# Optimization experiments

Measured on AMD Instinct MI355X. Metric: run time of the kernel, lower is better.

## Reference

```python
import jax, jax.numpy as jnp
import numpy as np
from jax import lax

NUM_CNNS = 300
INPUT_LEN = 608
NUM_CLASSES = 50
FILTER = 19
POOL = 7
HIDDEN = 100
BATCH = 256
L_CONV = INPUT_LEN - FILTER + 1          # 590
L_POOL = (L_CONV - POOL) // POOL + 1     # 84
EPS = 1e-5


def setup_inputs() -> dict:
    key = jax.random.key(0)
    ks = jax.random.split(key, 24)
    U, H = NUM_CNNS, HIDDEN
    d = {}
    d["x"] = jax.random.normal(ks[0], (BATCH, 4, INPUT_LEN), dtype=jnp.float32)
    # conv1: grouped Conv1d(4*U -> U, k=19, groups=U) on replicated input == dense Conv1d(4 -> U)
    d["w1"] = jax.random.normal(ks[1], (U, 4, FILTER), dtype=jnp.float32) * 0.1
    d["b1"] = jax.random.normal(ks[2], (U,), dtype=jnp.float32) * 0.05
    d["g1"] = jax.random.uniform(ks[3], (U,), dtype=jnp.float32, minval=0.5, maxval=1.5)
    d["be1"] = jax.random.normal(ks[4], (U,), dtype=jnp.float32) * 0.05
    d["m1"] = jax.random.normal(ks[5], (U,), dtype=jnp.float32) * 0.05
    d["v1"] = jax.random.uniform(ks[6], (U,), dtype=jnp.float32, minval=0.5, maxval=1.5)
    # grouped 1x1 conv: per-unit Linear 84 -> 100
    d["w2"] = jax.random.normal(ks[7], (U, H, L_POOL), dtype=jnp.float32) * (1.0 / np.sqrt(L_POOL))
    d["b2"] = jax.random.normal(ks[8], (U, H), dtype=jnp.float32) * 0.05
    d["g2"] = jax.random.uniform(ks[9], (U, H), dtype=jnp.float32, minval=0.5, maxval=1.5)
    d["be2"] = jax.random.normal(ks[10], (U, H), dtype=jnp.float32) * 0.05
    d["m2"] = jax.random.normal(ks[11], (U, H), dtype=jnp.float32) * 0.05
    d["v2"] = jax.random.uniform(ks[12], (U, H), dtype=jnp.float32, minval=0.5, maxval=1.5)
    # grouped 1x1 conv: per-unit Linear 100 -> 1
    d["w3"] = jax.random.normal(ks[13], (U, H), dtype=jnp.float32) * (1.0 / np.sqrt(H))
    d["b3"] = jax.random.normal(ks[14], (U,), dtype=jnp.float32) * 0.05
    d["g3"] = jax.random.uniform(ks[15], (U,), dtype=jnp.float32, minval=0.5, maxval=1.5)
    d["be3"] = jax.random.normal(ks[16], (U,), dtype=jnp.float32) * 0.05
    d["m3"] = jax.random.normal(ks[17], (U,), dtype=jnp.float32) * 0.05
    d["v3"] = jax.random.uniform(ks[18], (U,), dtype=jnp.float32, minval=0.5, maxval=1.5)
    # final Linear(U -> num_classes)
    d["wf"] = jax.random.normal(ks[19], (NUM_CLASSES, U), dtype=jnp.float32) * (1.0 / np.sqrt(U))
    d["bf"] = jax.random.normal(ks[20], (NUM_CLASSES,), dtype=jnp.float32) * 0.05
    return d


def _bn(y, g, be, m, v):
    return (y - m) * (g * lax.rsqrt(v + EPS)) + be


def reference(x, w1, b1, g1, be1, m1, v1, w2, b2, g2, be2, m2, v2,
              w3, b3, g3, be3, m3, v3, wf, bf):
    # conv1 (replicate + grouped conv == dense conv over 4 channels)
    y = lax.conv_general_dilated(x, w1, window_strides=(1,), padding='VALID',
                                 dimension_numbers=('NCH', 'OIH', 'NCH'))  # [B,U,590]
    y = y + b1[None, :, None]
    y = _bn(y, g1[None, :, None], be1[None, :, None], m1[None, :, None], v1[None, :, None])
    y = jnp.exp(y)  # ExpActivation
    # MaxPool1d(7,7): 590 -> 84 (uses first 588 positions)
    B = y.shape[0]
    y = y[:, :, :L_POOL * POOL].reshape(B, NUM_CNNS, L_POOL, POOL).max(axis=-1)  # [B,U,84]
    # per-unit MLP 84 -> 100 (grouped 1x1 conv) + BN + ReLU (dropout is eval-mode identity)
    h = jnp.einsum('buf,uof->buo', y, w2) + b2[None]  # [B,U,100]
    h = _bn(h, g2[None], be2[None], m2[None], v2[None])
    h = jax.nn.relu(h)
    # per-unit 100 -> 1 + BN + ReLU
    z = jnp.einsum('buo,uo->bu', h, w3) + b3[None]  # [B,U]
    z = _bn(z, g3[None], be3[None], m3[None], v3[None])
    z = jax.nn.relu(z)
    # final Linear
    return z @ wf.T + bf
```

## Files before the change

kernel.cpp:

```cpp
#include <hip/hip_runtime.h>
#include <hip/hip_bf16.h>

#define BATCH    256
#define NU       300
#define LIN      608
#define FILT     19
#define LPOOL    84
#define POOL     7
#define HID      100
#define NCLS     50
#define EPS      1e-5f
#define KP       96
#define NP       112
#define LDK      104
#define WROW     104
#define WBROWS   320
#define TCHUNK   112
#define MTN      19
#define CSTR     116

typedef __attribute__((ext_vector_type(8))) short short8;
typedef __attribute__((ext_vector_type(4))) float float4v;
typedef __attribute__((ext_vector_type(4))) unsigned short us4;

#define LDS_WAIT() __asm__ __volatile__("s_waitcnt lgkmcnt(0)" ::: "memory")

__device__ __forceinline__ unsigned short f2bf(float f) {
    unsigned u = __float_as_uint(f);
    u += 0x7fffu + ((u >> 16) & 1u);
    return (unsigned short)(u >> 16);
}
__device__ __forceinline__ float bf2f(unsigned short h) {
    return __uint_as_float(((unsigned)h) << 16);
}

__global__ void k_prep(const float* __restrict__ w1, const float* __restrict__ x,
                       const float* __restrict__ b1, const float* __restrict__ g1,
                       const float* __restrict__ be1, const float* __restrict__ m1,
                       const float* __restrict__ v1, const float* __restrict__ w2,
                       unsigned short* __restrict__ Wbh,
                       unsigned short* __restrict__ Wbl,
                       unsigned int* __restrict__ xc,
                       float2* __restrict__ s1c1,
                       unsigned short* __restrict__ w2c)
{
    const int idx = blockIdx.x * 256 + threadIdx.x;
    const int NW = WBROWS * WROW;
    if (idx < NW) {
        const int u = idx / WROW, kk = idx - u * WROW;
        float wv = 0.f;
        if (u < NU && kk < 96) {
            const int c = kk / 24, tap = kk - 24 * c;
            if (tap < FILT) wv = w1[(u * 4 + c) * FILT + tap];
        }
        const unsigned short hi = f2bf(wv);
        Wbh[idx] = hi;
        Wbl[idx] = f2bf(wv - bf2f(hi));
    }
    const int j = idx - NW;
    if (j >= 0 && j < BATCH * 4 * LIN) {
        const float xv = x[j];
        const unsigned short hi = f2bf(xv);
        const unsigned short lo = f2bf(xv - bf2f(hi));
        xc[j] = (unsigned)hi | ((unsigned)lo << 16);
    }
    const int j2 = j - BATCH * 4 * LIN;
    if (j2 >= 0 && j2 < MTN * 16) {
        float2 v = {0.f, 0.f};
        if (j2 < NU) {
            const float s = g1[j2] * rsqrtf(v1[j2] + EPS);
            v.x = s;
            v.y = (b1[j2] - m1[j2]) * s + be1[j2];
        }
        s1c1[j2] = v;
    }
    const int j3 = j2 - MTN * 16;
    if (j3 >= 0 && j3 < NU * NP * LDK) {
        const int u  = j3 / (NP * LDK);
        const int r  = j3 - u * (NP * LDK);
        const int o  = r / LDK;
        const int kc = r - o * LDK;
        float wv = 0.f;
        if (o < HID && kc < LPOOL) wv = w2[((size_t)u * HID + o) * LPOOL + kc];
        w2c[j3] = f2bf(wv);
    }
}

__global__ __launch_bounds__(256, 3)
void k_conv7d(const unsigned short* __restrict__ Wbh,
              const unsigned short* __restrict__ Wbl,
              const unsigned int* __restrict__ xc,
              const float2* __restrict__ s1c1,
              unsigned short* __restrict__ ypool)
{
    __shared__ __align__(16) unsigned short Bh[TCHUNK * LDK];
    __shared__ __align__(16) float Cs[4][16 * CSTR];

    const int tid = threadIdx.x;
    const int b   = blockIdx.x;
    const int tc  = blockIdx.y;
    const int t0  = TCHUNK * tc;
    const int NT  = (tc == 5) ? 2 : 7;

    for (int i = tid; i < TCHUNK * 12; i += 256) {
        const int trow = i / 12;
        if (trow >= 16 * NT) continue;
        const int rem   = i - 12 * trow;
        const int c     = rem / 3;
        const int third = rem - 3 * c;
        const int kkb   = 24 * c + 8 * third;
        const int tt0   = t0 + trow + 8 * third;
        const unsigned int* src = xc + ((b * 4 + c) * LIN + tt0);

        unsigned int w[8];
        if (third < 2 && tt0 + 8 <= LIN) {
            const uint4 v0 = *(const uint4*)(src);
            const uint4 v1 = *(const uint4*)(src + 4);
            w[0] = v0.x; w[1] = v0.y; w[2] = v0.z; w[3] = v0.w;
            w[4] = v1.x; w[5] = v1.y; w[6] = v1.z; w[7] = v1.w;
        } else {
#pragma unroll
            for (int j = 0; j < 8; ++j) {
                const int tap = 8 * third + j;
                const int tt  = tt0 + j;
                unsigned int v = 0;
                if (tap < FILT && tt < LIN) v = src[j];
                w[j] = v;
            }
        }
        short8 hv;
#pragma unroll
        for (int j = 0; j < 8; ++j) hv[j] = (short)(w[j] & 0xffffu);
        *(short8*)(&Bh[trow * LDK + kkb]) = hv;
    }
    __syncthreads();

    const int lane = tid & 63;
    const int n    = lane & 15;
    const int quad = lane >> 4;
    const int wave = tid >> 6;
    float* Csw = Cs[wave];

    const int u_l = lane & 15;
    const int wq  = lane >> 4;
    const int pg0 = 16 * tc + 4 * wq;

    const int jend = 5 * wave + ((wave == 3) ? 4 : 5);
    for (int mt0 = 5 * wave; mt0 < jend; mt0 += 2) {
        const bool two = (mt0 + 1 < jend);

        short8 a0h[3], a0l[3], a1h[3], a1l[3];
        {
            const unsigned short* wrh = Wbh + (size_t)(mt0 * 16 + n) * WROW;
            const unsigned short* wrl = Wbl + (size_t)(mt0 * 16 + n) * WROW;
#pragma unroll
            for (int s = 0; s < 3; ++s) {
                a0h[s] = *(const short8*)(wrh + 32 * s + 8 * quad);
                a0l[s] = *(const short8*)(wrl + 32 * s + 8 * quad);
            }
            const int m1r = two ? (mt0 + 1) : mt0;
            const unsigned short* wrh1 = Wbh + (size_t)(m1r * 16 + n) * WROW;
            const unsigned short* wrl1 = Wbl + (size_t)(m1r * 16 + n) * WROW;
#pragma unroll
            for (int s = 0; s < 3; ++s) {
                a1h[s] = *(const short8*)(wrh1 + 32 * s + 8 * quad);
                a1l[s] = *(const short8*)(wrl1 + 32 * s + 8 * quad);
            }
        }

        float4v acc[2][7];
#pragma unroll
        for (int t2 = 0; t2 < 2; ++t2)
#pragma unroll
            for (int nt = 0; nt < 7; ++nt)
                acc[t2][nt] = (float4v){0.f, 0.f, 0.f, 0.f};

#pragma unroll
        for (int nt = 0; nt < 7; ++nt) {
            if (nt < NT) {
                short8 bhf[3];
#pragma unroll
                for (int s = 0; s < 3; ++s)
                    bhf[s] = *(const short8*)(&Bh[(16 * nt + n) * LDK + 32 * s + 8 * quad]);
#pragma unroll
                for (int s = 0; s < 3; ++s)
                    acc[0][nt] = __builtin_amdgcn_mfma_f32_16x16x32_bf16(
                        bhf[s], a0h[s], acc[0][nt], 0, 0, 0);
#pragma unroll
                for (int s = 0; s < 3; ++s)
                    acc[0][nt] = __builtin_amdgcn_mfma_f32_16x16x32_bf16(
                        bhf[s], a0l[s], acc[0][nt], 0, 0, 0);
                if (two) {
#pragma unroll
                    for (int s = 0; s < 3; ++s)
                        acc[1][nt] = __builtin_amdgcn_mfma_f32_16x16x32_bf16(
                            bhf[s], a1h[s], acc[1][nt], 0, 0, 0);
#pragma unroll
                    for (int s = 0; s < 3; ++s)
                        acc[1][nt] = __builtin_amdgcn_mfma_f32_16x16x32_bf16(
                            bhf[s], a1l[s], acc[1][nt], 0, 0, 0);
                }
            }
        }

#pragma unroll
        for (int t2 = 0; t2 < 2; ++t2) {
            if (t2 == 1 && !two) break;
            const int mt = mt0 + t2;

            LDS_WAIT();
#pragma unroll
            for (int nt = 0; nt < 7; ++nt) {
                if (nt < NT)
                    *(float4v*)(&Csw[n * CSTR + 16 * nt + 4 * quad]) = acc[t2][nt];
            }
            LDS_WAIT();

            float rv[28];
#pragma unroll
            for (int r7 = 0; r7 < 7; ++r7)
                *(float4v*)(&rv[4 * r7]) =
                    *(const float4v*)(&Csw[u_l * CSTR + 28 * wq + 4 * r7]);

            const int uglob = mt * 16 + u_l;
            const float2 sc = s1c1[uglob];
            us4 pk;
#pragma unroll
            for (int w4 = 0; w4 < 4; ++w4) {
                const int pg = pg0 + w4;
                unsigned short ov = 0;
                if (pg < LPOOL) {
                    float m0 = fmaxf(rv[7 * w4 + 0], rv[7 * w4 + 1]);
                    float m1 = fmaxf(rv[7 * w4 + 2], rv[7 * w4 + 3]);
                    float m2 = fmaxf(rv[7 * w4 + 4], rv[7 * w4 + 5]);
                    m0 = fmaxf(m0, rv[7 * w4 + 6]);
                    ov = f2bf(__expf(fmaf(fmaxf(fmaxf(m0, m1), m2), sc.x, sc.y)));
                }
                pk[w4] = ov;
            }
            if (uglob < NU)
                *(us4*)(&ypool[((size_t)b * NU + uglob) * KP + pg0]) = pk;
        }
    }
}

__global__ __launch_bounds__(256, 4)
void k_mlp(const unsigned short* __restrict__ ypool,
           const unsigned short* __restrict__ w2c,
           const float* __restrict__ g2, const float* __restrict__ b2,
           const float* __restrict__ be2, const float* __restrict__ m2,
           const float* __restrict__ v2,
           const float* __restrict__ w3, const float* __restrict__ b3,
           const float* __restrict__ g3, const float* __restrict__ be3,
           const float* __restrict__ m3, const float* __restrict__ v3,
           float* __restrict__ zbuf)
{
    __shared__ __align__(16) float4 cs4[NP];

    const int tid = threadIdx.x;
    const int u   = blockIdx.x;
    const int b0  = blockIdx.y * 64;

    if (tid < NP) {
        float4 cv = {0.f, 0.f, 0.f, 0.f};
        if (tid < HID) {
            const int uo = u * HID + tid;
            const float s = g2[uo] * rsqrtf(v2[uo] + EPS);
            cv.x = s;
            cv.y = (b2[uo] - m2[uo]) * s + be2[uo];
            cv.z = w3[uo];
        }
        cs4[tid] = cv;
    }
    __syncthreads();

    const int lane = tid & 63;
    const int wave = tid >> 6;
    const int col  = lane & 15;
    const int quad = lane >> 4;
    const int bb   = b0 + 16 * wave + col;

    short8 bf_[3];
    {
        const unsigned short* yrow = ypool + ((size_t)bb * NU + u) * KP;
#pragma unroll
        for (int s = 0; s < 3; ++s)
            bf_[s] = *(const short8*)(yrow + 32 * s + 8 * quad);
    }

    const unsigned short* wbase = w2c + (size_t)u * (NP * LDK);
    float zp = 0.f;
#pragma unroll
    for (int mt = 0; mt < 7; ++mt) {
        short8 af[3];
#pragma unroll
        for (int s = 0; s < 3; ++s)
            af[s] = *(const short8*)(wbase + (16 * mt + col) * LDK + 32 * s + 8 * quad);

        float4v a0 = {0.f, 0.f, 0.f, 0.f};
#pragma unroll
        for (int s = 0; s < 3; ++s)
            a0 = __builtin_amdgcn_mfma_f32_16x16x32_bf16(af[s], bf_[s], a0, 0, 0, 0);
#pragma unroll
        for (int r = 0; r < 4; ++r) {
            const float4 cv = cs4[16 * mt + 4 * quad + r];
            zp = fmaf(fmaxf(fmaf(a0[r], cv.x, cv.y), 0.f), cv.z, zp);
        }
    }

    zp += __shfl_xor(zp, 16);
    zp += __shfl_xor(zp, 32);

    if (quad == 0) {
        const float s3 = g3[u] * rsqrtf(v3[u] + EPS);
        const float c3 = (b3[u] - m3[u]) * s3 + be3[u];
        zbuf[(size_t)u * BATCH + bb] = fmaxf(fmaf(zp, s3, c3), 0.f);
    }
}

__global__ __launch_bounds__(256, 4)
void k_final(const float* __restrict__ zbuf, const float* __restrict__ wf,
             const float* __restrict__ bf, float* __restrict__ out)
{
    __shared__ float red[4][64];
    const int nc   = blockIdx.x;
    const int bq   = blockIdx.y;
    const int lane = threadIdx.x & 63;
    const int wave = threadIdx.x >> 6;
    const int b    = bq * 64 + lane;

    float a0 = 0.f, a1 = 0.f, a2 = 0.f;
    const int u0 = wave * 75;
#pragma unroll 5
    for (int i = 0; i < 75; i += 3) {
        a0 = fmaf(zbuf[(size_t)(u0 + i + 0) * BATCH + b], wf[nc * NU + u0 + i + 0], a0);
        a1 = fmaf(zbuf[(size_t)(u0 + i + 1) * BATCH + b], wf[nc * NU + u0 + i + 1], a1);
        a2 = fmaf(zbuf[(size_t)(u0 + i + 2) * BATCH + b], wf[nc * NU + u0 + i + 2], a2);
    }
    red[wave][lane] = (a0 + a1) + a2;
    __syncthreads();
    if (threadIdx.x < 64) {
        const float s = (red[0][lane] + red[1][lane]) + (red[2][lane] + red[3][lane]);
        out[(size_t)b * NCLS + nc] = s + bf[nc];
    }
}

extern "C" void kernel_launch(void* const* d_in, const int* in_sizes, int n_in,
                              void* d_out, int out_size, void* d_ws, size_t ws_size,
                              hipStream_t stream)
{
    const float* x   = (const float*)d_in[0];
    const float* w1  = (const float*)d_in[1];
    const float* b1  = (const float*)d_in[2];
    const float* g1  = (const float*)d_in[3];
    const float* be1 = (const float*)d_in[4];
    const float* m1  = (const float*)d_in[5];
    const float* v1  = (const float*)d_in[6];
    const float* w2  = (const float*)d_in[7];
    const float* b2  = (const float*)d_in[8];
    const float* g2  = (const float*)d_in[9];
    const float* be2 = (const float*)d_in[10];
    const float* m2  = (const float*)d_in[11];
    const float* v2  = (const float*)d_in[12];
    const float* w3  = (const float*)d_in[13];
    const float* b3  = (const float*)d_in[14];
    const float* g3  = (const float*)d_in[15];
    const float* be3 = (const float*)d_in[16];
    const float* m3  = (const float*)d_in[17];
    const float* v3  = (const float*)d_in[18];
    const float* wf  = (const float*)d_in[19];
    const float* bf  = (const float*)d_in[20];

    unsigned short* ypool = (unsigned short*)d_ws;
    float* zbuf = (float*)((char*)d_ws + 14745600);
    unsigned short* Wbh = (unsigned short*)((char*)d_ws + 15052800);
    unsigned short* Wbl = (unsigned short*)((char*)d_ws + 15119360);
    unsigned int*   xc  = (unsigned int*)((char*)d_ws + 15185920);
    float2*         sc1 = (float2*)((char*)d_ws + 17676288);
    unsigned short* w2c = (unsigned short*)((char*)d_ws + 17678720);

    const int prep_elems = WBROWS * WROW + BATCH * 4 * LIN + MTN * 16 + NU * NP * LDK;
    k_prep<<<(prep_elems + 255) / 256, 256, 0, stream>>>(
        w1, x, b1, g1, be1, m1, v1, w2, Wbh, Wbl, xc, sc1, w2c);

    dim3 gc(BATCH, 6);
    k_conv7d<<<gc, 256, 0, stream>>>(Wbh, Wbl, xc, sc1, ypool);

    dim3 gm(NU, BATCH / 64);
    k_mlp<<<gm, 256, 0, stream>>>(ypool, w2c, g2, b2, be2, m2, v2,
                                  w3, b3, g3, be3, m3, v3, zbuf);

    dim3 gf(NCLS, 4);
    k_final<<<gf, 256, 0, stream>>>(zbuf, wf, bf, (float*)d_out);
}
```

Measured before the change: 150.7 us.

## Reuse w2 fragments across two batch tiles in MLP kernel, tighten w2 layout

The MLP kernel now processes 128 batch rows per block instead of 64. Each loaded weight fragment feeds two MFMA chains, which halves the global reads of the per-unit w2 tile, and the grid shrinks to 600 blocks. The packed w2 row stride is reduced from 104 to 96 to cut prep writes and the memory footprint. The conv kernel's staging loop is reindexed plane-major so consecutive threads read consecutive time rows, which should coalesce better. In exchange the MLP kernel uses more registers per thread and runs fewer blocks.

```diff
diff --git a/kernel.cpp b/kernel.cpp
--- a/kernel.cpp
+++ b/kernel.cpp
@@ -13,6 +13,7 @@
 #define KP       96
 #define NP       112
 #define LDK      104
+#define LDKW     96
 #define WROW     104
 #define WBROWS   320
 #define TCHUNK   112
@@ -75,11 +76,11 @@
         s1c1[j2] = v;
     }
     const int j3 = j2 - MTN * 16;
-    if (j3 >= 0 && j3 < NU * NP * LDK) {
-        const int u  = j3 / (NP * LDK);
-        const int r  = j3 - u * (NP * LDK);
-        const int o  = r / LDK;
-        const int kc = r - o * LDK;
+    if (j3 >= 0 && j3 < NU * NP * LDKW) {
+        const int u  = j3 / (NP * LDKW);
+        const int r  = j3 - u * (NP * LDKW);
+        const int o  = r / LDKW;
+        const int kc = r - o * LDKW;
         float wv = 0.f;
         if (o < HID && kc < LPOOL) wv = w2[((size_t)u * HID + o) * LPOOL + kc];
         w2c[j3] = f2bf(wv);
@@ -102,12 +103,12 @@
     const int t0  = TCHUNK * tc;
     const int NT  = (tc == 5) ? 2 : 7;
 
-    for (int i = tid; i < TCHUNK * 12; i += 256) {
-        const int trow = i / 12;
+    for (int i = tid; i < 12 * TCHUNK; i += 256) {
+        const int plane = i / TCHUNK;
+        const int trow  = i - plane * TCHUNK;
         if (trow >= 16 * NT) continue;
-        const int rem   = i - 12 * trow;
-        const int c     = rem / 3;
-        const int third = rem - 3 * c;
+        const int third = plane >> 2;
+        const int c     = plane & 3;
         const int kkb   = 24 * c + 8 * third;
         const int tt0   = t0 + trow + 8 * third;
         const unsigned int* src = xc + ((b * 4 + c) * LIN + tt0);
@@ -259,7 +260,7 @@
 
     const int tid = threadIdx.x;
     const int u   = blockIdx.x;
-    const int b0  = blockIdx.y * 64;
+    const int b0  = blockIdx.y * 128;
 
     if (tid < NP) {
         float4 cv = {0.f, 0.f, 0.f, 0.f};
@@ -278,43 +279,51 @@
     const int wave = tid >> 6;
     const int col  = lane & 15;
     const int quad = lane >> 4;
-    const int bb   = b0 + 16 * wave + col;
-
-    short8 bf_[3];
+    const int bbA  = b0 + 16 * wave + col;
+    const int bbB  = bbA + 64;
+
+    short8 bfA[3], bfB[3];
     {
-        const unsigned short* yrow = ypool + ((size_t)bb * NU + u) * KP;
-#pragma unroll
-        for (int s = 0; s < 3; ++s)
-            bf_[s] = *(const short8*)(yrow + 32 * s + 8 * quad);
-    }
-
-    const unsigned short* wbase = w2c + (size_t)u * (NP * LDK);
-    float zp = 0.f;
+        const unsigned short* yrA = ypool + ((size_t)bbA * NU + u) * KP;
+        const unsigned short* yrB = ypool + ((size_t)bbB * NU + u) * KP;
+#pragma unroll
+        for (int s = 0; s < 3; ++s) {
+            bfA[s] = *(const short8*)(yrA + 32 * s + 8 * quad);
+            bfB[s] = *(const short8*)(yrB + 32 * s + 8 * quad);
+        }
+    }
+
+    const unsigned short* wbase = w2c + (size_t)u * (NP * LDKW);
+    float zpA = 0.f, zpB = 0.f;
 #pragma unroll
     for (int mt = 0; mt < 7; ++mt) {
         short8 af[3];
 #pragma unroll
         for (int s = 0; s < 3; ++s)
-            af[s] = *(const short8*)(wbase + (16 * mt + col) * LDK + 32 * s + 8 * quad);
-
-        float4v a0 = {0.f, 0.f, 0.f, 0.f};
-#pragma unroll
-        for (int s = 0; s < 3; ++s)
-            a0 = __builtin_amdgcn_mfma_f32_16x16x32_bf16(af[s], bf_[s], a0, 0, 0, 0);
+            af[s] = *(const short8*)(wbase + (16 * mt + col) * LDKW + 32 * s + 8 * quad);
+
+        float4v a0 = {0.f, 0.f, 0.f, 0.f}, a1 = {0.f, 0.f, 0.f, 0.f};
+#pragma unroll
+        for (int s = 0; s < 3; ++s) {
+            a0 = __builtin_amdgcn_mfma_f32_16x16x32_bf16(af[s], bfA[s], a0, 0, 0, 0);
+            a1 = __builtin_amdgcn_mfma_f32_16x16x32_bf16(af[s], bfB[s], a1, 0, 0, 0);
+        }
 #pragma unroll
         for (int r = 0; r < 4; ++r) {
             const float4 cv = cs4[16 * mt + 4 * quad + r];
-            zp = fmaf(fmaxf(fmaf(a0[r], cv.x, cv.y), 0.f), cv.z, zp);
-        }
-    }
-
-    zp += __shfl_xor(zp, 16);
-    zp += __shfl_xor(zp, 32);
+            zpA = fmaf(fmaxf(fmaf(a0[r], cv.x, cv.y), 0.f), cv.z, zpA);
+            zpB = fmaf(fmaxf(fmaf(a1[r], cv.x, cv.y), 0.f), cv.z, zpB);
+        }
+    }
+
+    zpA += __shfl_xor(zpA, 16); zpA += __shfl_xor(zpA, 32);
+    zpB += __shfl_xor(zpB, 16); zpB += __shfl_xor(zpB, 32);
 
     if (quad == 0) {
         const float s3 = g3[u] * rsqrtf(v3[u] + EPS);
         const float c3 = (b3[u] - m3[u]) * s3 + be3[u];
-        zbuf[(size_t)u * BATCH + bb] = fmaxf(fmaf(zp, s3, c3), 0.f);
+        zbuf[(size_t)u * BATCH + bbA] = fmaxf(fmaf(zpA, s3, c3), 0.f);
+        zbuf[(size_t)u * BATCH + bbB] = fmaxf(fmaf(zpB, s3, c3), 0.f);
     }
 }
 
@@ -379,14 +388,14 @@
     float2*         sc1 = (float2*)((char*)d_ws + 17676288);
     unsigned short* w2c = (unsigned short*)((char*)d_ws + 17678720);
 
-    const int prep_elems = WBROWS * WROW + BATCH * 4 * LIN + MTN * 16 + NU * NP * LDK;
+    const int prep_elems = WBROWS * WROW + BATCH * 4 * LIN + MTN * 16 + NU * NP * LDKW;
     k_prep<<<(prep_elems + 255) / 256, 256, 0, stream>>>(
         w1, x, b1, g1, be1, m1, v1, w2, Wbh, Wbl, xc, sc1, w2c);
 
     dim3 gc(BATCH, 6);
     k_conv7d<<<gc, 256, 0, stream>>>(Wbh, Wbl, xc, sc1, ypool);
 
-    dim3 gm(NU, BATCH / 64);
+    dim3 gm(NU, 2);
     k_mlp<<<gm, 256, 0, stream>>>(ypool, w2c, g2, b2, be2, m2, v2,
                                   w3, b3, g3, be3, m3, v3, zbuf);
 
```

Measured after the change: 148.8 us (median of 2 runs). About the same (-1.3%).

## Fuse prep conversions into conv and MLP kernels, batch all rows per MLP block

Applied to the files above, without the earlier changes.

Removes the separate prep kernel that converted x, w1, w2 and the BN1 constants into bf16 workspace buffers. Conv now reads fp32 x and w1 directly, converts them inline, and computes the BN scale and shift itself. The MLP kernel reads fp32 w2 and converts it on the fly, and each block now handles all 256 batch rows (4 groups) so every w2 load is reused four times. This trades one launch plus a workspace round trip for redundant per-block conversion work, scattered scalar w1 loads, and only 300 MLP blocks instead of 1200, which lowers parallelism.

```diff
diff --git a/kernel.cpp b/kernel.cpp
--- a/kernel.cpp
+++ b/kernel.cpp
@@ -13,8 +13,6 @@
 #define KP       96
 #define NP       112
 #define LDK      104
-#define WROW     104
-#define WBROWS   320
 #define TCHUNK   112
 #define MTN      19
 #define CSTR     116
@@ -34,63 +32,12 @@
     return __uint_as_float(((unsigned)h) << 16);
 }
 
-__global__ void k_prep(const float* __restrict__ w1, const float* __restrict__ x,
-                       const float* __restrict__ b1, const float* __restrict__ g1,
-                       const float* __restrict__ be1, const float* __restrict__ m1,
-                       const float* __restrict__ v1, const float* __restrict__ w2,
-                       unsigned short* __restrict__ Wbh,
-                       unsigned short* __restrict__ Wbl,
-                       unsigned int* __restrict__ xc,
-                       float2* __restrict__ s1c1,
-                       unsigned short* __restrict__ w2c)
-{
-    const int idx = blockIdx.x * 256 + threadIdx.x;
-    const int NW = WBROWS * WROW;
-    if (idx < NW) {
-        const int u = idx / WROW, kk = idx - u * WROW;
-        float wv = 0.f;
-        if (u < NU && kk < 96) {
-            const int c = kk / 24, tap = kk - 24 * c;
-            if (tap < FILT) wv = w1[(u * 4 + c) * FILT + tap];
-        }
-        const unsigned short hi = f2bf(wv);
-        Wbh[idx] = hi;
-        Wbl[idx] = f2bf(wv - bf2f(hi));
-    }
-    const int j = idx - NW;
-    if (j >= 0 && j < BATCH * 4 * LIN) {
-        const float xv = x[j];
-        const unsigned short hi = f2bf(xv);
-        const unsigned short lo = f2bf(xv - bf2f(hi));
-        xc[j] = (unsigned)hi | ((unsigned)lo << 16);
-    }
-    const int j2 = j - BATCH * 4 * LIN;
-    if (j2 >= 0 && j2 < MTN * 16) {
-        float2 v = {0.f, 0.f};
-        if (j2 < NU) {
-            const float s = g1[j2] * rsqrtf(v1[j2] + EPS);
-            v.x = s;
-            v.y = (b1[j2] - m1[j2]) * s + be1[j2];
-        }
-        s1c1[j2] = v;
-    }
-    const int j3 = j2 - MTN * 16;
-    if (j3 >= 0 && j3 < NU * NP * LDK) {
-        const int u  = j3 / (NP * LDK);
-        const int r  = j3 - u * (NP * LDK);
-        const int o  = r / LDK;
-        const int kc = r - o * LDK;
-        float wv = 0.f;
-        if (o < HID && kc < LPOOL) wv = w2[((size_t)u * HID + o) * LPOOL + kc];
-        w2c[j3] = f2bf(wv);
-    }
-}
-
 __global__ __launch_bounds__(256, 3)
-void k_conv7d(const unsigned short* __restrict__ Wbh,
-              const unsigned short* __restrict__ Wbl,
-              const unsigned int* __restrict__ xc,
-              const float2* __restrict__ s1c1,
+void k_conv7d(const float* __restrict__ x,
+              const float* __restrict__ w1,
+              const float* __restrict__ b1, const float* __restrict__ g1,
+              const float* __restrict__ be1, const float* __restrict__ m1,
+              const float* __restrict__ v1,
               unsigned short* __restrict__ ypool)
 {
     __shared__ __align__(16) unsigned short Bh[TCHUNK * LDK];
@@ -102,20 +49,20 @@
     const int t0  = TCHUNK * tc;
     const int NT  = (tc == 5) ? 2 : 7;
 
-    for (int i = tid; i < TCHUNK * 12; i += 256) {
-        const int trow = i / 12;
+    for (int i = tid; i < 12 * TCHUNK; i += 256) {
+        const int plane = i / TCHUNK;
+        const int trow  = i - plane * TCHUNK;
         if (trow >= 16 * NT) continue;
-        const int rem   = i - 12 * trow;
-        const int c     = rem / 3;
-        const int third = rem - 3 * c;
+        const int third = plane >> 2;
+        const int c     = plane & 3;
         const int kkb   = 24 * c + 8 * third;
         const int tt0   = t0 + trow + 8 * third;
-        const unsigned int* src = xc + ((b * 4 + c) * LIN + tt0);
-
-        unsigned int w[8];
+        const float* src = x + ((b * 4 + c) * LIN + tt0);
+
+        float w[8];
         if (third < 2 && tt0 + 8 <= LIN) {
-            const uint4 v0 = *(const uint4*)(src);
-            const uint4 v1 = *(const uint4*)(src + 4);
+            const float4 v0 = *(const float4*)(src);
+            const float4 v1 = *(const float4*)(src + 4);
             w[0] = v0.x; w[1] = v0.y; w[2] = v0.z; w[3] = v0.w;
             w[4] = v1.x; w[5] = v1.y; w[6] = v1.z; w[7] = v1.w;
         } else {
@@ -123,14 +70,14 @@
             for (int j = 0; j < 8; ++j) {
                 const int tap = 8 * third + j;
                 const int tt  = tt0 + j;
-                unsigned int v = 0;
+                float v = 0.f;
                 if (tap < FILT && tt < LIN) v = src[j];
                 w[j] = v;
             }
         }
         short8 hv;
 #pragma unroll
-        for (int j = 0; j < 8; ++j) hv[j] = (short)(w[j] & 0xffffu);
+        for (int j = 0; j < 8; ++j) hv[j] = (short)f2bf(w[j]);
         *(short8*)(&Bh[trow * LDK + kkb]) = hv;
     }
     __syncthreads();
@@ -145,28 +92,40 @@
     const int wq  = lane >> 4;
     const int pg0 = 16 * tc + 4 * wq;
 
+    int woff[3][8];
+#pragma unroll
+    for (int s = 0; s < 3; ++s)
+#pragma unroll
+        for (int j = 0; j < 8; ++j) {
+            const int kk  = 32 * s + 8 * quad + j;
+            const int c   = kk / 24;
+            const int tap = kk - 24 * c;
+            woff[s][j] = (tap < FILT) ? (c * FILT + tap) : -1;
+        }
+
+    auto loadW = [&](short8 (&ah)[3], short8 (&al)[3], int mt) {
+        const int u = mt * 16 + n;
+        const bool uv = (u < NU);
+        const float* wr = w1 + u * (4 * FILT);
+#pragma unroll
+        for (int s = 0; s < 3; ++s)
+#pragma unroll
+            for (int j = 0; j < 8; ++j) {
+                const int o = woff[s][j];
+                float wv = (uv && o >= 0) ? wr[o] : 0.f;
+                const unsigned short hi = f2bf(wv);
+                ah[s][j] = (short)hi;
+                al[s][j] = (short)f2bf(wv - bf2f(hi));
+            }
+    };
+
     const int jend = 5 * wave + ((wave == 3) ? 4 : 5);
     for (int mt0 = 5 * wave; mt0 < jend; mt0 += 2) {
         const bool two = (mt0 + 1 < jend);
 
         short8 a0h[3], a0l[3], a1h[3], a1l[3];
-        {
-            const unsigned short* wrh = Wbh + (size_t)(mt0 * 16 + n) * WROW;
-            const unsigned short* wrl = Wbl + (size_t)(mt0 * 16 + n) * WROW;
-#pragma unroll
-            for (int s = 0; s < 3; ++s) {
-                a0h[s] = *(const short8*)(wrh + 32 * s + 8 * quad);
-                a0l[s] = *(const short8*)(wrl + 32 * s + 8 * quad);
-            }
-            const int m1r = two ? (mt0 + 1) : mt0;
-            const unsigned short* wrh1 = Wbh + (size_t)(m1r * 16 + n) * WROW;
-            const unsigned short* wrl1 = Wbl + (size_t)(m1r * 16 + n) * WROW;
-#pragma unroll
-            for (int s = 0; s < 3; ++s) {
-                a1h[s] = *(const short8*)(wrh1 + 32 * s + 8 * quad);
-                a1l[s] = *(const short8*)(wrl1 + 32 * s + 8 * quad);
-            }
-        }
+        loadW(a0h, a0l, mt0);
+        loadW(a1h, a1l, two ? (mt0 + 1) : mt0);
 
         float4v acc[2][7];
 #pragma unroll
@@ -223,7 +182,12 @@
                     *(const float4v*)(&Csw[u_l * CSTR + 28 * wq + 4 * r7]);
 
             const int uglob = mt * 16 + u_l;
-            const float2 sc = s1c1[uglob];
+            float scx = 0.f, scy = 0.f;
+            if (uglob < NU) {
+                const float s1 = g1[uglob] * rsqrtf(v1[uglob] + EPS);
+                scx = s1;
+                scy = (b1[uglob] - m1[uglob]) * s1 + be1[uglob];
+            }
             us4 pk;
 #pragma unroll
             for (int w4 = 0; w4 < 4; ++w4) {
@@ -231,10 +195,10 @@
                 unsigned short ov = 0;
                 if (pg < LPOOL) {
                     float m0 = fmaxf(rv[7 * w4 + 0], rv[7 * w4 + 1]);
-                    float m1 = fmaxf(rv[7 * w4 + 2], rv[7 * w4 + 3]);
+                    float m1x = fmaxf(rv[7 * w4 + 2], rv[7 * w4 + 3]);
                     float m2 = fmaxf(rv[7 * w4 + 4], rv[7 * w4 + 5]);
                     m0 = fmaxf(m0, rv[7 * w4 + 6]);
-                    ov = f2bf(__expf(fmaf(fmaxf(fmaxf(m0, m1), m2), sc.x, sc.y)));
+                    ov = f2bf(__expf(fmaf(fmaxf(fmaxf(m0, m1x), m2), scx, scy)));
                 }
                 pk[w4] = ov;
             }
@@ -246,7 +210,7 @@
 
 __global__ __launch_bounds__(256, 4)
 void k_mlp(const unsigned short* __restrict__ ypool,
-           const unsigned short* __restrict__ w2c,
+           const float* __restrict__ w2,
            const float* __restrict__ g2, const float* __restrict__ b2,
            const float* __restrict__ be2, const float* __restrict__ m2,
            const float* __restrict__ v2,
@@ -259,7 +223,6 @@
 
     const int tid = threadIdx.x;
     const int u   = blockIdx.x;
-    const int b0  = blockIdx.y * 64;
 
     if (tid < NP) {
         float4 cv = {0.f, 0.f, 0.f, 0.f};
@@ -278,43 +241,83 @@
     const int wave = tid >> 6;
     const int col  = lane & 15;
     const int quad = lane >> 4;
-    const int bb   = b0 + 16 * wave + col;
-
-    short8 bf_[3];
-    {
-        const unsigned short* yrow = ypool + ((size_t)bb * NU + u) * KP;
+
+    short8 bf_[4][3];
+#pragma unroll
+    for (int g = 0; g < 4; ++g) {
+        const int bb = 64 * g + 16 * wave + col;
+        const unsigned short* yr = ypool + ((size_t)bb * NU + u) * KP;
 #pragma unroll
         for (int s = 0; s < 3; ++s)
-            bf_[s] = *(const short8*)(yrow + 32 * s + 8 * quad);
-    }
-
-    const unsigned short* wbase = w2c + (size_t)u * (NP * LDK);
-    float zp = 0.f;
+            bf_[g][s] = *(const short8*)(yr + 32 * s + 8 * quad);
+    }
+
+    const float* wb = w2 + (size_t)u * HID * LPOOL;
+    float zp[4] = {0.f, 0.f, 0.f, 0.f};
 #pragma unroll
     for (int mt = 0; mt < 7; ++mt) {
+        const int o = 16 * mt + col;
         short8 af[3];
+        if (o < HID) {
+            const float* row = wb + o * LPOOL;
+#pragma unroll
+            for (int s = 0; s < 3; ++s) {
+                const int kk0 = 32 * s + 8 * quad;
+                float v[8];
+                if (kk0 <= 76) {
+                    const float4 p0 = *(const float4*)(row + kk0);
+                    const float4 p1 = *(const float4*)(row + kk0 + 4);
+                    v[0] = p0.x; v[1] = p0.y; v[2] = p0.z; v[3] = p0.w;
+                    v[4] = p1.x; v[5] = p1.y; v[6] = p1.z; v[7] = p1.w;
+                } else if (kk0 == 80) {
+                    const float4 p0 = *(const float4*)(row + 80);
+                    v[0] = p0.x; v[1] = p0.y; v[2] = p0.z; v[3] = p0.w;
+                    v[4] = 0.f; v[5] = 0.f; v[6] = 0.f; v[7] = 0.f;
+                } else {
+#pragma unroll
+                    for (int j = 0; j < 8; ++j) v[j] = 0.f;
+                }
+#pragma unroll
+                for (int j = 0; j < 8; ++j) af[s][j] = (short)f2bf(v[j]);
+            }
+        } else {
+#pragma unroll
+            for (int s = 0; s < 3; ++s)
+#pragma unroll
+                for (int j = 0; j < 8; ++j) af[s][j] = 0;
+        }
+
+        float4v a[4];
+#pragma unroll
+        for (int g = 0; g < 4; ++g) a[g] = (float4v){0.f, 0.f, 0.f, 0.f};
 #pragma unroll
         for (int s = 0; s < 3; ++s)
-            af[s] = *(const short8*)(wbase + (16 * mt + col) * LDK + 32 * s + 8 * quad);
-
-        float4v a0 = {0.f, 0.f, 0.f, 0.f};
-#pragma unroll
-        for (int s = 0; s < 3; ++s)
-            a0 = __builtin_amdgcn_mfma_f32_16x16x32_bf16(af[s], bf_[s], a0, 0, 0, 0);
+#pragma unroll
+            for (int g = 0; g < 4; ++g)
+                a[g] = __builtin_amdgcn_mfma_f32_16x16x32_bf16(af[s], bf_[g][s], a[g], 0, 0, 0);
 #pragma unroll
         for (int r = 0; r < 4; ++r) {
             const float4 cv = cs4[16 * mt + 4 * quad + r];
-            zp = fmaf(fmaxf(fmaf(a0[r], cv.x, cv.y), 0.f), cv.z, zp);
-        }
-    }
-
-    zp += __shfl_xor(zp, 16);
-    zp += __shfl_xor(zp, 32);
+#pragma unroll
+            for (int g = 0; g < 4; ++g)
+                zp[g] = fmaf(fmaxf(fmaf(a[g][r], cv.x, cv.y), 0.f), cv.z, zp[g]);
+        }
+    }
+
+#pragma unroll
+    for (int g = 0; g < 4; ++g) {
+        zp[g] += __shfl_xor(zp[g], 16);
+        zp[g] += __shfl_xor(zp[g], 32);
+    }
 
     if (quad == 0) {
         const float s3 = g3[u] * rsqrtf(v3[u] + EPS);
         const float c3 = (b3[u] - m3[u]) * s3 + be3[u];
-        zbuf[(size_t)u * BATCH + bb] = fmaxf(fmaf(zp, s3, c3), 0.f);
+#pragma unroll
+        for (int g = 0; g < 4; ++g) {
+            const int bb = 64 * g + 16 * wave + col;
+            zbuf[(size_t)u * BATCH + bb] = fmaxf(fmaf(zp[g], s3, c3), 0.f);
+        }
     }
 }
 
@@ -373,21 +376,11 @@
 
     unsigned short* ypool = (unsigned short*)d_ws;
     float* zbuf = (float*)((char*)d_ws + 14745600);
-    unsigned short* Wbh = (unsigned short*)((char*)d_ws + 15052800);
-    unsigned short* Wbl = (unsigned short*)((char*)d_ws + 15119360);
-    unsigned int*   xc  = (unsigned int*)((char*)d_ws + 15185920);
-    float2*         sc1 = (float2*)((char*)d_ws + 17676288);
-    unsigned short* w2c = (unsigned short*)((char*)d_ws + 17678720);
-
-    const int prep_elems = WBROWS * WROW + BATCH * 4 * LIN + MTN * 16 + NU * NP * LDK;
-    k_prep<<<(prep_elems + 255) / 256, 256, 0, stream>>>(
-        w1, x, b1, g1, be1, m1, v1, w2, Wbh, Wbl, xc, sc1, w2c);
 
     dim3 gc(BATCH, 6);
-    k_conv7d<<<gc, 256, 0, stream>>>(Wbh, Wbl, xc, sc1, ypool);
-
-    dim3 gm(NU, BATCH / 64);
-    k_mlp<<<gm, 256, 0, stream>>>(ypool, w2c, g2, b2, be2, m2, v2,
+    k_conv7d<<<gc, 256, 0, stream>>>(x, w1, b1, g1, be1, m1, v1, ypool);
+
+    k_mlp<<<NU, 256, 0, stream>>>(ypool, w2, g2, b2, be2, m2, v2,
                                   w3, b3, g3, be3, m3, v3, zbuf);
 
     dim3 gf(NCLS, 4);
```

Result: slower. 216.1 us (+43.4%).
